# Kernel optimization log

Measured on AMD Instinct MI355X. Metric: run time of the kernel, lower is better.

Reference implementation:

```python
import jax, jax.numpy as jnp
import numpy as np

N, C = 1048576, 64
EPS = 1e-5          # bn eps
ACOSH_EPS = 1e-7    # clamp arccosh arg > 1


def linner(u, v):
    """Lorentz inner product <u,v>_L = -u0*v0 + sum_i ui*vi, keepdims on last axis."""
    p = u * v
    return -p[..., :1] + jnp.sum(p[..., 1:], axis=-1, keepdims=True)


def setup_inputs() -> dict:
    key = jax.random.key(0)
    k1, = jax.random.split(key, 1)
    # sample spatial coords, project onto hyperboloid: x0 = sqrt(1 + ||xs||^2)  (k=1)
    xs = jax.random.normal(k1, (N, C - 1), dtype=jnp.float32) * 0.2
    x0 = jnp.sqrt(1.0 + jnp.sum(xs * xs, axis=-1, keepdims=True))
    x = jnp.concatenate([x0, xs], axis=-1)                      # [N, C] on manifold
    gamma = jnp.ones((1,), dtype=jnp.float32)
    beta = jnp.zeros((C,), dtype=jnp.float32).at[0].set(1.0)    # manifold origin
    return {"x": x, "gamma": gamma, "beta": beta}


def reference(x, gamma, beta):
    # ---- 1. Lorentzian centroid (Frechet mean, k=1) ----
    s = jnp.mean(x, axis=0)                                     # [C]
    sn = jnp.sqrt(jnp.clip(-linner(s, s), 1e-9))                # sqrt(-<s,s>_L)
    mu = s / sn                                                 # [C], on manifold
    mu_b = mu[None, :]                                          # [1, C]

    # ---- 2. distance + variance in tangent space ----
    alpha = jnp.clip(-linner(x, mu_b), 1.0 + ACOSH_EPS)         # [N,1], -<x,mu>_L
    d = jnp.arccosh(alpha)                                      # [N,1]
    var = jnp.mean(d * d)
    div = jnp.sqrt(var + EPS)

    # ---- 3. logmap at mu: d/sqrt(a^2-1) * (x - a*mu) ----
    u = x - alpha * mu_b                                        # [N, C]
    v = (d / jnp.sqrt(jnp.clip(alpha * alpha - 1.0, ACOSH_EPS))) * u

    # ---- 4. parallel transport mu -> origin o=(1,0,...) ----
    # PT_{p->q}(v) = v + <q,v>_L / (1 - <p,q>_L) * (p + q)
    o = jnp.zeros((C,), dtype=x.dtype).at[0].set(1.0)
    ov = -v[..., :1]                                            # <o,v>_L
    denom_mo = 1.0 - (-mu[0])                                   # 1 - <mu,o>_L
    v = v + (ov / denom_mo) * (mu_b + o[None, :])

    # ---- 5. scale ----
    v = v * (gamma / div)

    # ---- 6. transport origin -> beta ----
    bv = linner(beta[None, :], v)                               # [N,1]
    denom_ob = 1.0 - (-beta[0])                                 # 1 - <o,beta>_L
    v = v + (bv / denom_ob) * (o + beta)[None, :]

    # ---- 7. expmap at beta ----
    vn = jnp.sqrt(jnp.clip(linner(v, v), 1e-9))                 # [N,1] tangent norm
    out = jnp.cosh(vn) * beta[None, :] + jnp.sinh(vn) * (v / vn)
    return out
```

## Files before the change

kernel.cpp:

```cpp
#include <hip/hip_runtime.h>
#include <math.h>

#define NROWS 1048576
#define C 64
#define GRID 4096
#define BLOCK 256
#define GPT ((GRID * BLOCK) / 16)
#define NITER (NROWS / GPT)

constexpr float EPS = 1e-5f;
constexpr float ACOSH_EPS = 1e-7f;


__device__ __forceinline__ float row16_sum(float x) {
    x += __int_as_float(__builtin_amdgcn_update_dpp(
        0, __float_as_int(x), 0x121, 0xF, 0xF, true));
    x += __int_as_float(__builtin_amdgcn_update_dpp(
        0, __float_as_int(x), 0x122, 0xF, 0xF, true));
    x += __int_as_float(__builtin_amdgcn_update_dpp(
        0, __float_as_int(x), 0x124, 0xF, 0xF, true));
    x += __int_as_float(__builtin_amdgcn_update_dpp(
        0, __float_as_int(x), 0x128, 0xF, 0xF, true));
    return x;
}

__global__ __launch_bounds__(BLOCK) void colsum_kernel(
    const float* __restrict__ x, float* __restrict__ ws) {
    const int tid = threadIdx.x;
    const int g = tid & 15;
    const int gid0 = (blockIdx.x * BLOCK + tid) >> 4;
    const float* p = x + (size_t)gid0 * C + g * 4;
    float4 a0 = {0, 0, 0, 0}, a1 = {0, 0, 0, 0}, a2 = {0, 0, 0, 0}, a3 = {0, 0, 0, 0};
    #pragma unroll
    for (int k = 0; k < NITER; k += 4) {
        const float4 v0 = *(const float4*)(p + (size_t)(k + 0) * GPT * C);
        const float4 v1 = *(const float4*)(p + (size_t)(k + 1) * GPT * C);
        const float4 v2 = *(const float4*)(p + (size_t)(k + 2) * GPT * C);
        const float4 v3 = *(const float4*)(p + (size_t)(k + 3) * GPT * C);
        a0.x += v0.x; a0.y += v0.y; a0.z += v0.z; a0.w += v0.w;
        a1.x += v1.x; a1.y += v1.y; a1.z += v1.z; a1.w += v1.w;
        a2.x += v2.x; a2.y += v2.y; a2.z += v2.z; a2.w += v2.w;
        a3.x += v3.x; a3.y += v3.y; a3.z += v3.z; a3.w += v3.w;
    }
    float4 acc;
    acc.x = (a0.x + a1.x) + (a2.x + a3.x);
    acc.y = (a0.y + a1.y) + (a2.y + a3.y);
    acc.z = (a0.z + a1.z) + (a2.z + a3.z);
    acc.w = (a0.w + a1.w) + (a2.w + a3.w);
    #pragma unroll
    for (int m = 16; m <= 32; m <<= 1) {
        acc.x += __shfl_xor(acc.x, m, 64);
        acc.y += __shfl_xor(acc.y, m, 64);
        acc.z += __shfl_xor(acc.z, m, 64);
        acc.w += __shfl_xor(acc.w, m, 64);
    }
    __shared__ float lsum[4][64];
    const int wave = tid >> 6, lane = tid & 63;
    if (lane < 16) {
        lsum[wave][lane * 4 + 0] = acc.x;
        lsum[wave][lane * 4 + 1] = acc.y;
        lsum[wave][lane * 4 + 2] = acc.z;
        lsum[wave][lane * 4 + 3] = acc.w;
    }
    __syncthreads();
    if (tid < 64) {
        const float s = lsum[0][tid] + lsum[1][tid] + lsum[2][tid] + lsum[3][tid];
        atomicAdd(&ws[tid], s);
    }
}

__global__ void mu_kernel(float* __restrict__ ws) {
    const int j = threadIdx.x;
    const float s = ws[j] * (1.0f / (float)NROWS);
    float p = s * s;
    if (j == 0) p = -p;
    #pragma unroll
    for (int m = 1; m < 64; m <<= 1) p += __shfl_xor(p, m, 64);
    const float sn = sqrtf(fmaxf(-p, 1e-9f));
    ws[64 + j] = s / sn;
}

__global__ __launch_bounds__(BLOCK) void var_kernel(
    const float* __restrict__ x, float* __restrict__ ws) {
    const int tid = threadIdx.x;
    const int g = tid & 15;
    const int gid0 = (blockIdx.x * BLOCK + tid) >> 4;
    float4 smu = *(const float4*)(ws + 64 + g * 4);
    if (g == 0) smu.x = -smu.x;
    float dacc = 0.f;
    #pragma unroll 8
    for (int k = 0; k < NITER; ++k) {
        const size_t r = (size_t)gid0 + (size_t)(NITER - 1 - k) * GPT;
        const float4 v = *(const float4*)(x + r * C + g * 4);
        float p = fmaf(v.x, smu.x, fmaf(v.y, smu.y, fmaf(v.z, smu.z, v.w * smu.w)));
        p = row16_sum(p);
        const float alpha = fmaxf(-p, 1.0f + ACOSH_EPS);
        const float t = fmaf(alpha, alpha, -1.0f);
        const float d = __logf(alpha + sqrtf(t));
        dacc = fmaf(d, d, dacc);
    }
    dacc = row16_sum(dacc);
    dacc += __shfl_xor(dacc, 16, 64);
    dacc += __shfl_xor(dacc, 32, 64);
    __shared__ float wsum[4];
    const int wave = tid >> 6, lane = tid & 63;
    if (lane == 0) wsum[wave] = dacc;
    __syncthreads();
    if (tid == 0)
        atomicAdd(&ws[128], (wsum[0] + wsum[1] + wsum[2] + wsum[3]) * (1.0f / 16.0f));
}

__global__ __launch_bounds__(BLOCK) void out_kernel(
    const float* __restrict__ x, const float* __restrict__ gamma,
    const float* __restrict__ beta, float* __restrict__ out,
    const float* __restrict__ ws) {
    const int tid = threadIdx.x;
    const int g = tid & 15;
    const int gid0 = (blockIdx.x * BLOCK + tid) >> 4;
    const float4 muv = *(const float4*)(ws + 64 + g * 4);
    const float4 bev = *(const float4*)(beta + g * 4);
    float4 smu = muv, sbe = bev;
    if (g == 0) { smu.x = -smu.x; sbe.x = -sbe.x; }
    const float e0 = (g == 0) ? 1.0f : 0.0f;
    const float mu0 = ws[64];
    const float beta0 = beta[0];
    const float var = ws[128] * (1.0f / (float)NROWS);
    const float divv = sqrtf(var + EPS);
    const float gscale = gamma[0] / divv;
    const float inv_dmo = 1.0f / (1.0f + mu0);
    const float inv_dob = 1.0f / (1.0f + beta0);
    #pragma unroll 4
    for (int k = 0; k < NITER; ++k) {
        const size_t r = (size_t)gid0 + (size_t)k * GPT;
        const float4 xv = *(const float4*)(x + r * C + g * 4);
        float p = fmaf(xv.x, smu.x, fmaf(xv.y, smu.y, fmaf(xv.z, smu.z, xv.w * smu.w)));
        float x0m = (g == 0) ? xv.x : 0.0f;
        p = row16_sum(p);
        const float x0 = row16_sum(x0m);
        const float alpha = fmaxf(-p, 1.0f + ACOSH_EPS);
        const float t = fmaf(alpha, alpha, -1.0f);
        const float sq = sqrtf(t);
        const float d = __logf(alpha + sq);
        const float f = d * rsqrtf(fmaxf(t, ACOSH_EPS));
        float4 v;
        v.x = f * fmaf(-alpha, muv.x, xv.x);
        v.y = f * fmaf(-alpha, muv.y, xv.y);
        v.z = f * fmaf(-alpha, muv.z, xv.z);
        v.w = f * fmaf(-alpha, muv.w, xv.w);
        const float v0 = f * fmaf(-alpha, mu0, x0);
        const float c1 = -v0 * inv_dmo;
        v.x = fmaf(c1, muv.x + e0, v.x);
        v.y = fmaf(c1, muv.y, v.y);
        v.z = fmaf(c1, muv.z, v.z);
        v.w = fmaf(c1, muv.w, v.w);
        v.x *= gscale; v.y *= gscale; v.z *= gscale; v.w *= gscale;
        float bv = fmaf(v.x, sbe.x, fmaf(v.y, sbe.y, fmaf(v.z, sbe.z, v.w * sbe.w)));
        bv = row16_sum(bv);
        const float c2 = bv * inv_dob;
        v.x = fmaf(c2, bev.x + e0, v.x);
        v.y = fmaf(c2, bev.y, v.y);
        v.z = fmaf(c2, bev.z, v.z);
        v.w = fmaf(c2, bev.w, v.w);
        const float svx = (g == 0) ? -v.x : v.x;
        float nn = fmaf(v.x, svx, fmaf(v.y, v.y, fmaf(v.z, v.z, v.w * v.w)));
        nn = row16_sum(nn);
        const float vn = sqrtf(fmaxf(nn, 1e-9f));
        const float e = __expf(vn);
        const float ei = __builtin_amdgcn_rcpf(e);
        const float ch = 0.5f * (e + ei);
        const float sc = 0.5f * (e - ei) * __builtin_amdgcn_rcpf(vn);
        float4 o;
        o.x = fmaf(sc, v.x, ch * bev.x);
        o.y = fmaf(sc, v.y, ch * bev.y);
        o.z = fmaf(sc, v.z, ch * bev.z);
        o.w = fmaf(sc, v.w, ch * bev.w);
        *(float4*)(out + r * C + g * 4) = o;
    }
}

extern "C" void kernel_launch(void* const* d_in, const int* in_sizes, int n_in,
                              void* d_out, int out_size, void* d_ws, size_t ws_size,
                              hipStream_t stream) {
    const float* x = (const float*)d_in[0];
    const float* gamma = (const float*)d_in[1];
    const float* beta = (const float*)d_in[2];
    float* out = (float*)d_out;
    float* ws = (float*)d_ws;

    hipMemsetAsync(ws, 0, 129 * sizeof(float), stream);
    colsum_kernel<<<GRID, BLOCK, 0, stream>>>(x, ws);
    mu_kernel<<<1, 64, 0, stream>>>(ws);
    var_kernel<<<GRID, BLOCK, 0, stream>>>(x, ws);
    out_kernel<<<GRID, BLOCK, 0, stream>>>(x, gamma, beta, out, ws);
}
```

Before: 608.8 us.

## Fuse all three passes into one cooperative kernel with grid syncs

Replaces the four separate launches (column sum, mu, variance, output) with a single cooperative kernel of 1024 blocks. Grid-wide syncs separate the phases, and every block recomputes mu locally. This removes launch gaps and may let parts of x (256 MB) stay in the large last-level cache between passes. It also uses nontemporal stores for the output. The risks are grid-sync cost, lower parallelism per pass, and fallback to the old path if the cooperative launch fails.

```diff
diff --git a/kernel.cpp b/kernel.cpp
--- a/kernel.cpp
+++ b/kernel.cpp
@@ -1,8 +1,17 @@
 #include <hip/hip_runtime.h>
+#include <hip/hip_cooperative_groups.h>
 #include <math.h>
+
+namespace cg = cooperative_groups;
 
 #define NROWS 1048576
 #define C 64
+
+#define FGRID 1024
+#define FBLOCK 256
+#define FRPS ((FGRID * FBLOCK) / 16)
+#define FNITER (NROWS / FRPS)
+
 #define GRID 4096
 #define BLOCK 256
 #define GPT ((GRID * BLOCK) / 16)
@@ -10,6 +19,8 @@
 
 constexpr float EPS = 1e-5f;
 constexpr float ACOSH_EPS = 1e-7f;
+
+typedef float f4 __attribute__((ext_vector_type(4)));
 
 
 __device__ __forceinline__ float row16_sum(float x) {
@@ -22,6 +33,170 @@
     x += __int_as_float(__builtin_amdgcn_update_dpp(
         0, __float_as_int(x), 0x128, 0xF, 0xF, true));
     return x;
+}
+
+__global__ __launch_bounds__(FBLOCK, 4) void lbn_fused(
+    const float* __restrict__ x, const float* __restrict__ gamma,
+    const float* __restrict__ beta, float* __restrict__ out,
+    float* __restrict__ ws) {
+    cg::grid_group gg = cg::this_grid();
+    const int tid = threadIdx.x;
+    const int g = tid & 15;
+    const int gid0 = ((int)blockIdx.x * FBLOCK + tid) >> 4;
+    const int wave = tid >> 6, lane = tid & 63;
+    __shared__ float lsum[4][64];
+    __shared__ float wsum[4];
+
+    {
+        const float* p = x + (size_t)gid0 * C + g * 4;
+        float4 a0{0, 0, 0, 0}, a1{0, 0, 0, 0}, a2{0, 0, 0, 0}, a3{0, 0, 0, 0};
+        #pragma unroll 2
+        for (int k = 0; k < FNITER; k += 4) {
+            const float4 v0 = *(const float4*)(p + (size_t)(k + 0) * FRPS * C);
+            const float4 v1 = *(const float4*)(p + (size_t)(k + 1) * FRPS * C);
+            const float4 v2 = *(const float4*)(p + (size_t)(k + 2) * FRPS * C);
+            const float4 v3 = *(const float4*)(p + (size_t)(k + 3) * FRPS * C);
+            a0.x += v0.x; a0.y += v0.y; a0.z += v0.z; a0.w += v0.w;
+            a1.x += v1.x; a1.y += v1.y; a1.z += v1.z; a1.w += v1.w;
+            a2.x += v2.x; a2.y += v2.y; a2.z += v2.z; a2.w += v2.w;
+            a3.x += v3.x; a3.y += v3.y; a3.z += v3.z; a3.w += v3.w;
+        }
+        float4 acc;
+        acc.x = (a0.x + a1.x) + (a2.x + a3.x);
+        acc.y = (a0.y + a1.y) + (a2.y + a3.y);
+        acc.z = (a0.z + a1.z) + (a2.z + a3.z);
+        acc.w = (a0.w + a1.w) + (a2.w + a3.w);
+        #pragma unroll
+        for (int m = 16; m <= 32; m <<= 1) {
+            acc.x += __shfl_xor(acc.x, m, 64);
+            acc.y += __shfl_xor(acc.y, m, 64);
+            acc.z += __shfl_xor(acc.z, m, 64);
+            acc.w += __shfl_xor(acc.w, m, 64);
+        }
+        if (lane < 16) {
+            lsum[wave][lane * 4 + 0] = acc.x;
+            lsum[wave][lane * 4 + 1] = acc.y;
+            lsum[wave][lane * 4 + 2] = acc.z;
+            lsum[wave][lane * 4 + 3] = acc.w;
+        }
+        __syncthreads();
+        if (tid < 64) {
+            const float s = lsum[0][tid] + lsum[1][tid] + lsum[2][tid] + lsum[3][tid];
+            atomicAdd(&ws[tid], s);
+        }
+    }
+    __threadfence();
+    gg.sync();
+
+    const float invN = 1.0f / (float)NROWS;
+    float4 muv;
+    float mu0;
+    {
+        float4 sv = *(const float4*)(ws + g * 4);
+        sv.x *= invN; sv.y *= invN; sv.z *= invN; sv.w *= invN;
+        float pp = fmaf(sv.y, sv.y, fmaf(sv.z, sv.z, sv.w * sv.w));
+        pp = (g == 0) ? fmaf(-sv.x, sv.x, pp) : fmaf(sv.x, sv.x, pp);
+        pp = row16_sum(pp);
+        const float sn = sqrtf(fmaxf(-pp, 1e-9f));
+        const float inv_sn = 1.0f / sn;
+        muv.x = sv.x * inv_sn; muv.y = sv.y * inv_sn;
+        muv.z = sv.z * inv_sn; muv.w = sv.w * inv_sn;
+        mu0 = ws[0] * invN * inv_sn;
+    }
+    float4 smu = muv;
+    if (g == 0) smu.x = -smu.x;
+
+    {
+        float dacc0 = 0.f, dacc1 = 0.f;
+        #pragma unroll 2
+        for (int k = 0; k < FNITER; k += 2) {
+            const size_t r0 = (size_t)gid0 + (size_t)(FNITER - 1 - k) * FRPS;
+            const size_t r1 = (size_t)gid0 + (size_t)(FNITER - 2 - k) * FRPS;
+            const float4 v0 = *(const float4*)(x + r0 * C + g * 4);
+            const float4 v1 = *(const float4*)(x + r1 * C + g * 4);
+            float p0 = fmaf(v0.x, smu.x, fmaf(v0.y, smu.y, fmaf(v0.z, smu.z, v0.w * smu.w)));
+            float p1 = fmaf(v1.x, smu.x, fmaf(v1.y, smu.y, fmaf(v1.z, smu.z, v1.w * smu.w)));
+            p0 = row16_sum(p0);
+            p1 = row16_sum(p1);
+            const float al0 = fmaxf(-p0, 1.0f + ACOSH_EPS);
+            const float al1 = fmaxf(-p1, 1.0f + ACOSH_EPS);
+            const float t0 = fmaf(al0, al0, -1.0f);
+            const float t1 = fmaf(al1, al1, -1.0f);
+            const float d0 = __logf(al0 + sqrtf(t0));
+            const float d1 = __logf(al1 + sqrtf(t1));
+            dacc0 = fmaf(d0, d0, dacc0);
+            dacc1 = fmaf(d1, d1, dacc1);
+        }
+        float dacc = dacc0 + dacc1;
+        dacc = row16_sum(dacc);
+        dacc += __shfl_xor(dacc, 16, 64);
+        dacc += __shfl_xor(dacc, 32, 64);
+        if (lane == 0) wsum[wave] = dacc;
+        __syncthreads();
+        if (tid == 0)
+            atomicAdd(&ws[128], (wsum[0] + wsum[1] + wsum[2] + wsum[3]) * (1.0f / 16.0f));
+    }
+    __threadfence();
+    gg.sync();
+
+    {
+        const float4 bev = *(const float4*)(beta + g * 4);
+        float4 sbe = bev;
+        if (g == 0) sbe.x = -sbe.x;
+        const float e0 = (g == 0) ? 1.0f : 0.0f;
+        const float beta0 = beta[0];
+        const float var = ws[128] * invN;
+        const float divv = sqrtf(var + EPS);
+        const float gscale = gamma[0] / divv;
+        const float inv_dmo = 1.0f / (1.0f + mu0);
+        const float inv_dob = 1.0f / (1.0f + beta0);
+        for (int k = 0; k < FNITER; ++k) {
+            const size_t r = (size_t)gid0 + (size_t)k * FRPS;
+            const float4 xv = *(const float4*)(x + r * C + g * 4);
+            float p = fmaf(xv.x, smu.x, fmaf(xv.y, smu.y, fmaf(xv.z, smu.z, xv.w * smu.w)));
+            float x0m = (g == 0) ? xv.x : 0.0f;
+            p = row16_sum(p);
+            const float x0 = row16_sum(x0m);
+            const float alpha = fmaxf(-p, 1.0f + ACOSH_EPS);
+            const float t = fmaf(alpha, alpha, -1.0f);
+            const float sq = sqrtf(t);
+            const float d = __logf(alpha + sq);
+            const float f = d * rsqrtf(fmaxf(t, ACOSH_EPS));
+            float4 v;
+            v.x = f * fmaf(-alpha, muv.x, xv.x);
+            v.y = f * fmaf(-alpha, muv.y, xv.y);
+            v.z = f * fmaf(-alpha, muv.z, xv.z);
+            v.w = f * fmaf(-alpha, muv.w, xv.w);
+            const float v0 = f * fmaf(-alpha, mu0, x0);
+            const float c1 = -v0 * inv_dmo;
+            v.x = fmaf(c1, muv.x + e0, v.x);
+            v.y = fmaf(c1, muv.y, v.y);
+            v.z = fmaf(c1, muv.z, v.z);
+            v.w = fmaf(c1, muv.w, v.w);
+            v.x *= gscale; v.y *= gscale; v.z *= gscale; v.w *= gscale;
+            float bv = fmaf(v.x, sbe.x, fmaf(v.y, sbe.y, fmaf(v.z, sbe.z, v.w * sbe.w)));
+            bv = row16_sum(bv);
+            const float c2 = bv * inv_dob;
+            v.x = fmaf(c2, bev.x + e0, v.x);
+            v.y = fmaf(c2, bev.y, v.y);
+            v.z = fmaf(c2, bev.z, v.z);
+            v.w = fmaf(c2, bev.w, v.w);
+            const float svx = (g == 0) ? -v.x : v.x;
+            float nn = fmaf(v.x, svx, fmaf(v.y, v.y, fmaf(v.z, v.z, v.w * v.w)));
+            nn = row16_sum(nn);
+            const float vn = sqrtf(fmaxf(nn, 1e-9f));
+            const float e = __expf(vn);
+            const float ei = __builtin_amdgcn_rcpf(e);
+            const float ch = 0.5f * (e + ei);
+            const float sc = 0.5f * (e - ei) * __builtin_amdgcn_rcpf(vn);
+            float4 o;
+            o.x = fmaf(sc, v.x, ch * bev.x);
+            o.y = fmaf(sc, v.y, ch * bev.y);
+            o.z = fmaf(sc, v.z, ch * bev.z);
+            o.w = fmaf(sc, v.w, ch * bev.w);
+            __builtin_nontemporal_store(*(const f4*)&o, (f4*)(out + r * C + g * 4));
+        }
+    }
 }
 
 __global__ __launch_bounds__(BLOCK) void colsum_kernel(
@@ -188,8 +363,14 @@
     float* ws = (float*)d_ws;
 
     hipMemsetAsync(ws, 0, 129 * sizeof(float), stream);
-    colsum_kernel<<<GRID, BLOCK, 0, stream>>>(x, ws);
-    mu_kernel<<<1, 64, 0, stream>>>(ws);
-    var_kernel<<<GRID, BLOCK, 0, stream>>>(x, ws);
-    out_kernel<<<GRID, BLOCK, 0, stream>>>(x, gamma, beta, out, ws);
-}
+
+    void* args[] = {(void*)&x, (void*)&gamma, (void*)&beta, (void*)&out, (void*)&ws};
+    hipError_t err = hipLaunchCooperativeKernel((const void*)lbn_fused, dim3(FGRID),
+                                                dim3(FBLOCK), args, 0, stream);
+    if (err != hipSuccess) {
+        colsum_kernel<<<GRID, BLOCK, 0, stream>>>(x, ws);
+        mu_kernel<<<1, 64, 0, stream>>>(ws);
+        var_kernel<<<GRID, BLOCK, 0, stream>>>(x, ws);
+        out_kernel<<<GRID, BLOCK, 0, stream>>>(x, gamma, beta, out, ws);
+    }
+}
```

Measured after the change: 1.006 ms. 1.65x slower.

## Remove mu kernel, spread atomics over 8 slots, nontemporal output stores

Applied to the files above, without the earlier changes.

Drops the single-block mu kernel. Each block of the var and out kernels now recomputes mu redundantly from eight partial column-sum slots. The column-sum and variance atomics are spread across eight slots keyed by block index to reduce atomic contention on the same addresses. Output stores become nontemporal to avoid polluting cache. The trade-off is extra per-block setup work reading the partial slots and a larger memset.

```diff
diff --git a/kernel.cpp b/kernel.cpp
--- a/kernel.cpp
+++ b/kernel.cpp
@@ -11,6 +11,9 @@
 constexpr float EPS = 1e-5f;
 constexpr float ACOSH_EPS = 1e-7f;
 
+typedef float f4 __attribute__((ext_vector_type(4)));
+
+#define WS_D2 512
 
 __device__ __forceinline__ float row16_sum(float x) {
     x += __int_as_float(__builtin_amdgcn_update_dpp(
@@ -22,6 +25,29 @@
     x += __int_as_float(__builtin_amdgcn_update_dpp(
         0, __float_as_int(x), 0x128, 0xF, 0xF, true));
     return x;
+}
+
+__device__ __forceinline__ void compute_mu(const float* __restrict__ ws, int g,
+                                           float4& muv, float& mu0) {
+    float4 sv = {0.f, 0.f, 0.f, 0.f};
+    #pragma unroll
+    for (int rep = 0; rep < 8; ++rep) {
+        const float4 t = *(const float4*)(ws + rep * 64 + g * 4);
+        sv.x += t.x; sv.y += t.y; sv.z += t.z; sv.w += t.w;
+    }
+    const float invN = 1.0f / (float)NROWS;
+    sv.x *= invN; sv.y *= invN; sv.z *= invN; sv.w *= invN;
+    float pp = fmaf(sv.y, sv.y, fmaf(sv.z, sv.z, sv.w * sv.w));
+    pp = (g == 0) ? fmaf(-sv.x, sv.x, pp) : fmaf(sv.x, sv.x, pp);
+    pp = row16_sum(pp);
+    const float sn = sqrtf(fmaxf(-pp, 1e-9f));
+    const float inv_sn = 1.0f / sn;
+    muv.x = sv.x * inv_sn; muv.y = sv.y * inv_sn;
+    muv.z = sv.z * inv_sn; muv.w = sv.w * inv_sn;
+    float s0 = 0.f;
+    #pragma unroll
+    for (int rep = 0; rep < 8; ++rep) s0 += ws[rep * 64];
+    mu0 = s0 * invN * inv_sn;
 }
 
 __global__ __launch_bounds__(BLOCK) void colsum_kernel(
@@ -65,19 +91,8 @@
     __syncthreads();
     if (tid < 64) {
         const float s = lsum[0][tid] + lsum[1][tid] + lsum[2][tid] + lsum[3][tid];
-        atomicAdd(&ws[tid], s);
-    }
-}
-
-__global__ void mu_kernel(float* __restrict__ ws) {
-    const int j = threadIdx.x;
-    const float s = ws[j] * (1.0f / (float)NROWS);
-    float p = s * s;
-    if (j == 0) p = -p;
-    #pragma unroll
-    for (int m = 1; m < 64; m <<= 1) p += __shfl_xor(p, m, 64);
-    const float sn = sqrtf(fmaxf(-p, 1e-9f));
-    ws[64 + j] = s / sn;
+        atomicAdd(&ws[(blockIdx.x & 7) * 64 + tid], s);
+    }
 }
 
 __global__ __launch_bounds__(BLOCK) void var_kernel(
@@ -85,7 +100,9 @@
     const int tid = threadIdx.x;
     const int g = tid & 15;
     const int gid0 = (blockIdx.x * BLOCK + tid) >> 4;
-    float4 smu = *(const float4*)(ws + 64 + g * 4);
+    float4 muv; float mu0;
+    compute_mu(ws, g, muv, mu0);
+    float4 smu = muv;
     if (g == 0) smu.x = -smu.x;
     float dacc = 0.f;
     #pragma unroll 8
@@ -107,7 +124,8 @@
     if (lane == 0) wsum[wave] = dacc;
     __syncthreads();
     if (tid == 0)
-        atomicAdd(&ws[128], (wsum[0] + wsum[1] + wsum[2] + wsum[3]) * (1.0f / 16.0f));
+        atomicAdd(&ws[WS_D2 + (blockIdx.x & 7)],
+                  (wsum[0] + wsum[1] + wsum[2] + wsum[3]) * (1.0f / 16.0f));
 }
 
 __global__ __launch_bounds__(BLOCK) void out_kernel(
@@ -117,14 +135,17 @@
     const int tid = threadIdx.x;
     const int g = tid & 15;
     const int gid0 = (blockIdx.x * BLOCK + tid) >> 4;
-    const float4 muv = *(const float4*)(ws + 64 + g * 4);
+    float4 muv; float mu0;
+    compute_mu(ws, g, muv, mu0);
     const float4 bev = *(const float4*)(beta + g * 4);
     float4 smu = muv, sbe = bev;
     if (g == 0) { smu.x = -smu.x; sbe.x = -sbe.x; }
     const float e0 = (g == 0) ? 1.0f : 0.0f;
-    const float mu0 = ws[64];
     const float beta0 = beta[0];
-    const float var = ws[128] * (1.0f / (float)NROWS);
+    float d2 = 0.f;
+    #pragma unroll
+    for (int rep = 0; rep < 8; ++rep) d2 += ws[WS_D2 + rep];
+    const float var = d2 * (1.0f / (float)NROWS);
     const float divv = sqrtf(var + EPS);
     const float gscale = gamma[0] / divv;
     const float inv_dmo = 1.0f / (1.0f + mu0);
@@ -174,7 +195,7 @@
         o.y = fmaf(sc, v.y, ch * bev.y);
         o.z = fmaf(sc, v.z, ch * bev.z);
         o.w = fmaf(sc, v.w, ch * bev.w);
-        *(float4*)(out + r * C + g * 4) = o;
+        __builtin_nontemporal_store(*(const f4*)&o, (f4*)(out + r * C + g * 4));
     }
 }
 
@@ -187,9 +208,8 @@
     float* out = (float*)d_out;
     float* ws = (float*)d_ws;
 
-    hipMemsetAsync(ws, 0, 129 * sizeof(float), stream);
+    hipMemsetAsync(ws, 0, 520 * sizeof(float), stream);
     colsum_kernel<<<GRID, BLOCK, 0, stream>>>(x, ws);
-    mu_kernel<<<1, 64, 0, stream>>>(ws);
     var_kernel<<<GRID, BLOCK, 0, stream>>>(x, ws);
     out_kernel<<<GRID, BLOCK, 0, stream>>>(x, gamma, beta, out, ws);
 }
```

New measurement: 561.4 us. -7.8%, faster.
